# Optimization experiments

Hardware: AMD Instinct MI355X
Metric: run time of the kernel (lower is better)

The kernel has to match this reference:

```python
import jax, jax.numpy as jnp
import numpy as np

B, S, H, NH = 2, 2048, 1024, 16
PH = H // NH  # per-head size = 64


def setup_inputs() -> dict:
    key = jax.random.key(0)
    ks = jax.random.split(key, 12)
    scale = 0.02
    inp = {
        "key": jax.random.normal(ks[0], (B, S, H), jnp.float32),
        "value": jax.random.normal(ks[1], (B, S, H), jnp.float32),
        "query": jax.random.normal(ks[2], (B, S, H), jnp.float32),
        "mask": jax.random.uniform(ks[3], (B, 1, S, S), jnp.float32),
        "i": 0,
        "Wq": jax.random.normal(ks[4], (H, H), jnp.float32) * scale,
        "bq": jnp.zeros((H,), jnp.float32),
        "Wk": jax.random.normal(ks[5], (H, H), jnp.float32) * scale,
        "bk": jnp.zeros((H,), jnp.float32),
        "Wv": jax.random.normal(ks[6], (H, H), jnp.float32) * scale,
        "bv": jnp.zeros((H,), jnp.float32),
        "Wo": jax.random.normal(ks[7], (H, H), jnp.float32) * scale,
        "bo": jnp.zeros((H,), jnp.float32),
    }
    return inp


def reference(key, value, query, mask, i, Wq, bq, Wk, bk, Wv, bv, Wo, bo):
    # Linear projections (torch nn.Linear: x @ W.T + b), then split heads -> [B, NH, S, PH]
    def proj(x, W, b):
        return (x @ W.T + b).reshape(B, S, NH, PH).transpose(0, 2, 1, 3)

    q = proj(query, Wq, bq)
    k = proj(key, Wk, bk)
    v = proj(value, Wv, bv)

    # scores: [B, NH, S, S]; scale then MULTIPLICATIVE mask (as in the original)
    scores = jnp.einsum('bhqd,bhkd->bhqk', q, k) / jnp.sqrt(jnp.float32(PH))
    scores = scores * mask
    probs = jax.nn.softmax(scores, axis=-1)  # dropout p=0 -> identity

    # context: [B, NH, S, PH] -> merge heads -> [B, S, H]
    ctx = jnp.einsum('bhqk,bhkd->bhqd', probs, v)
    ctx = ctx.transpose(0, 2, 1, 3).reshape(B, S, H)
    return ctx @ Wo.T + bo
```

## Files before the change

### kernel.cpp

```cpp
#include <hip/hip_runtime.h>

typedef unsigned short ushort_t;
typedef __attribute__((ext_vector_type(8))) __bf16 bf16x8;
typedef __attribute__((ext_vector_type(4))) float f32x4;

__device__ inline float bf2f(ushort_t u) {
  union { unsigned int i; float f; } v; v.i = ((unsigned int)u) << 16; return v.f;
}
__device__ inline ushort_t f2bf(float f) {
  union { float f; unsigned int i; } v; v.f = f;
  unsigned int r = (v.i + 0x7fffu + ((v.i >> 16) & 1u)) >> 16;
  return (ushort_t)r;
}

__global__ void detect_dtype_kernel(const ushort_t* __restrict__ w,
                                    int* __restrict__ flag) {
  if (threadIdx.x == 0 && blockIdx.x == 0) {
    int sane = 0;
    for (int i = 0; i < 256; i++) {
      float a = fabsf(bf2f(w[i]));
      if (a >= 1e-4f && a <= 0.5f) sane++;
    }
    *flag = (sane >= 192) ? 1 : 0;
  }
}

__device__ inline float ld1(const void* src, size_t idx, int isbf) {
  return isbf ? bf2f(((const ushort_t*)src)[idx]) : ((const float*)src)[idx];
}

struct pre8 { float4 a, b; };
__device__ inline pre8 pref8(const void* src, size_t idx, int isbf) {
  pre8 u;
  if (isbf) {
    u.a = *(const float4*)((const ushort_t*)src + idx);
    u.b = u.a;
  } else {
    const float* s = (const float*)src + idx;
    u.a = *(const float4*)s;
    u.b = *(const float4*)(s + 4);
  }
  return u;
}
__device__ inline void commit8(ushort_t* dst, pre8 u, int isbf) {
  if (isbf) {
    *(float4*)dst = u.a;
  } else {
    union { bf16x8 v; ushort_t u8[8]; } t;
    t.u8[0] = f2bf(u.a.x); t.u8[1] = f2bf(u.a.y); t.u8[2] = f2bf(u.a.z); t.u8[3] = f2bf(u.a.w);
    t.u8[4] = f2bf(u.b.x); t.u8[5] = f2bf(u.b.y); t.u8[6] = f2bf(u.b.z); t.u8[7] = f2bf(u.b.w);
    *(bf16x8*)dst = t.v;
  }
}
__device__ inline void cvt8(ushort_t* dst, const void* src, size_t idx, int isbf) {
  commit8(dst, pref8(src, idx, isbf), isbf);
}

#define NW_ ((size_t)1024 * 1024)
#define NX_ ((size_t)4096 * 1024)
#define NM_ ((size_t)2 * 2048 * 2048)

__global__ __launch_bounds__(256) void cvt_all_kernel(
    const void* xq, const void* xk, const void* xv,
    const void* wq, const void* wk, const void* wv, const void* wo,
    const void* mask, ushort_t* __restrict__ dst,
    const int* __restrict__ flag) {
  int seg = blockIdx.z;
  const void* src; size_t n, doff;
  switch (seg) {
    case 0: src = wq;   n = NW_; doff = 0;                 break;
    case 1: src = wk;   n = NW_; doff = NW_;               break;
    case 2: src = wv;   n = NW_; doff = 2 * NW_;           break;
    case 3: src = wo;   n = NW_; doff = 3 * NW_;           break;
    case 4: src = xq;   n = NX_; doff = 4 * NW_;           break;
    case 5: src = xk;   n = NX_; doff = 4 * NW_ + NX_;     break;
    case 6: src = xv;   n = NX_; doff = 4 * NW_ + 2 * NX_; break;
    default: src = mask; n = NM_; doff = 4 * NW_ + 3 * NX_; break;
  }
  size_t i = ((size_t)blockIdx.x * 256 + threadIdx.x) * 8;
  if (i >= n) return;
  cvt8(&dst[doff + i], src, i, *flag);
}

#define KDIM 1024
#define NDIM 1024

__device__ __forceinline__ void gld_lds16(ushort_t* lds, const ushort_t* g) {
  __builtin_amdgcn_global_load_lds(
      (const __attribute__((address_space(1))) void*)g,
      (__attribute__((address_space(3))) void*)lds, 16, 0, 0);
}

template <int MODE>
__global__ __launch_bounds__(256) void gemm_fast_kernel(
    const ushort_t* __restrict__ X0, const ushort_t* __restrict__ X1,
    const ushort_t* __restrict__ X2,
    const ushort_t* __restrict__ W0, const ushort_t* __restrict__ W1,
    const ushort_t* __restrict__ W2,
    const void* __restrict__ B0, const void* __restrict__ B1,
    const void* __restrict__ B2,
    void* __restrict__ O0, void* __restrict__ O1, void* __restrict__ O2,
    const int* __restrict__ flag) {
  __shared__ ushort_t As[128 * 64];
  __shared__ ushort_t Bs[128 * 64];
  const int z = blockIdx.z;
  const ushort_t* X = z == 0 ? X0 : z == 1 ? X1 : X2;
  const ushort_t* W = z == 0 ? W0 : z == 1 ? W1 : W2;
  const void* Bias  = z == 0 ? B0 : z == 1 ? B1 : B2;
  void* Out         = z == 0 ? O0 : z == 1 ? O1 : O2;
  const int f = *flag;

  const int tid = threadIdx.x;
  const int wave = tid >> 6, lane = tid & 63;
  const int g = lane >> 4, l16 = lane & 15;
  const int m0 = blockIdx.y * 128, n0 = blockIdx.x * 128;
  const int wm = (wave >> 1) * 64, wn = (wave & 1) * 64;
  const int lr = lane >> 3;
  const int lc = (lane & 7) ^ lr;

  f32x4 acc[4][4] = {};

  for (int k0 = 0; k0 < KDIM; k0 += 64) {
#pragma unroll
    for (int q = 0; q < 4; q++) {
      const int row = wave * 32 + q * 8;
      gld_lds16(&As[row * 64],
                &X[(size_t)(m0 + row + lr) * KDIM + k0 + lc * 8]);
      gld_lds16(&Bs[row * 64],
                &W[(size_t)(n0 + row + lr) * KDIM + k0 + lc * 8]);
    }
    __syncthreads();

    bf16x8 af[2][4], bfr[2][4];
#pragma unroll
    for (int kk = 0; kk < 2; kk++)
#pragma unroll
      for (int i = 0; i < 4; i++) {
        const int cs = ((g + 4 * kk) ^ (l16 & 7)) * 8;
        af[kk][i]  = *(const bf16x8*)&As[(wm + i * 16 + l16) * 64 + cs];
        bfr[kk][i] = *(const bf16x8*)&Bs[(wn + i * 16 + l16) * 64 + cs];
      }
#pragma unroll
    for (int kk = 0; kk < 2; kk++)
#pragma unroll
      for (int i = 0; i < 4; i++)
#pragma unroll
        for (int j = 0; j < 4; j++)
          acc[i][j] = __builtin_amdgcn_mfma_f32_16x16x32_bf16(
              af[kk][i], bfr[kk][j], acc[i][j], 0, 0, 0);
    __syncthreads();
  }

  for (int i = 0; i < 4; i++)
    for (int j = 0; j < 4; j++)
      for (int r = 0; r < 4; r++) {
        int m = m0 + wm + i * 16 + g * 4 + r;
        int n = n0 + wn + j * 16 + l16;
        float v = acc[i][j][r] + ld1(Bias, n, f);
        if (MODE == 0) {
          if (f) ((ushort_t*)Out)[(size_t)m * NDIM + n] = f2bf(v);
          else   ((float*)Out)[(size_t)m * NDIM + n] = v;
        } else {
          int b = m >> 11, s = m & 2047, h = n >> 6, d = n & 63;
          ((ushort_t*)Out)[((((size_t)b * 16 + h) * 2048) + s) * 64 + d] = f2bf(v);
        }
      }
}

#define BK 32

template <int MODE>
__device__ inline void gemm_body(const void* __restrict__ X,
                                 const void* __restrict__ W,
                                 const void* __restrict__ Bias,
                                 void* __restrict__ Out,
                                 int xbf, int wbf, int bbf, int obf) {
  __shared__ ushort_t As[128][BK + 8];
  __shared__ ushort_t Bs[128][BK + 8];
  const int tid = threadIdx.x;
  const int wave = tid >> 6, lane = tid & 63;
  const int g = lane >> 4, l16 = lane & 15;
  const int m0 = blockIdx.y * 128, n0 = blockIdx.x * 128;
  const int wm = (wave >> 1) * 64, wn = (wave & 1) * 64;

  f32x4 acc[4][4] = {};
  const int r0 = tid >> 2, c0 = (tid & 3) * 8;
  const size_t ia0 = (size_t)(m0 + r0) * KDIM + c0;
  const size_t ia1 = (size_t)(m0 + r0 + 64) * KDIM + c0;
  const size_t ib0 = (size_t)(n0 + r0) * KDIM + c0;
  const size_t ib1 = (size_t)(n0 + r0 + 64) * KDIM + c0;

  pre8 pa0 = pref8(X, ia0, xbf), pa1 = pref8(X, ia1, xbf);
  pre8 pb0 = pref8(W, ib0, wbf), pb1 = pref8(W, ib1, wbf);

  for (int k0 = 0; k0 < KDIM; k0 += BK) {
    commit8(&As[r0][c0],      pa0, xbf);
    commit8(&As[r0 + 64][c0], pa1, xbf);
    commit8(&Bs[r0][c0],      pb0, wbf);
    commit8(&Bs[r0 + 64][c0], pb1, wbf);
    const int kn = (k0 + BK) & (KDIM - 1);
    pa0 = pref8(X, ia0 + kn, xbf); pa1 = pref8(X, ia1 + kn, xbf);
    pb0 = pref8(W, ib0 + kn, wbf); pb1 = pref8(W, ib1 + kn, wbf);
    __syncthreads();
    bf16x8 af[4], bfr[4];
    for (int i = 0; i < 4; i++) af[i]  = *(const bf16x8*)&As[wm + i * 16 + l16][g * 8];
    for (int j = 0; j < 4; j++) bfr[j] = *(const bf16x8*)&Bs[wn + j * 16 + l16][g * 8];
    for (int i = 0; i < 4; i++)
      for (int j = 0; j < 4; j++)
        acc[i][j] = __builtin_amdgcn_mfma_f32_16x16x32_bf16(af[i], bfr[j], acc[i][j], 0, 0, 0);
    __syncthreads();
  }
  for (int i = 0; i < 4; i++)
    for (int j = 0; j < 4; j++)
      for (int r = 0; r < 4; r++) {
        int m = m0 + wm + i * 16 + g * 4 + r;
        int n = n0 + wn + j * 16 + l16;
        float v = acc[i][j][r] + ld1(Bias, n, bbf);
        if (MODE == 0) {
          if (obf) ((ushort_t*)Out)[(size_t)m * NDIM + n] = f2bf(v);
          else     ((float*)Out)[(size_t)m * NDIM + n] = v;
        } else {
          int b = m >> 11, s = m & 2047, h = n >> 6, d = n & 63;
          ((ushort_t*)Out)[((((size_t)b * 16 + h) * 2048) + s) * 64 + d] = f2bf(v);
        }
      }
}

__global__ __launch_bounds__(256) void proj_qkv_fb_kernel(
    const void* __restrict__ query, const void* __restrict__ key,
    const void* __restrict__ value,
    const void* __restrict__ Wq, const void* __restrict__ bq,
    const void* __restrict__ Wk, const void* __restrict__ bk,
    const void* __restrict__ Wv, const void* __restrict__ bv,
    ushort_t* __restrict__ Q, ushort_t* __restrict__ K, ushort_t* __restrict__ V,
    const int* __restrict__ flag) {
  int f = *flag;
  int z = blockIdx.z;
  const void* X = z == 0 ? query : z == 1 ? key : value;
  const void* W = z == 0 ? Wq : z == 1 ? Wk : Wv;
  const void* B = z == 0 ? bq : z == 1 ? bk : bv;
  ushort_t* O  = z == 0 ? Q  : z == 1 ? K  : V;
  gemm_body<1>(X, W, B, O, f, f, f, 1);
}

__global__ __launch_bounds__(256) void out_proj_fb_kernel(
    const ushort_t* __restrict__ X, const void* __restrict__ W,
    const void* __restrict__ B, void* __restrict__ O,
    const int* __restrict__ flag) {
  int f = *flag;
  gemm_body<0>(X, W, B, O, 1, f, f, f);
}

__global__ __launch_bounds__(256) void transpose_v_kernel(
    const ushort_t* __restrict__ Vin, ushort_t* __restrict__ Vout) {
  __shared__ ushort_t T[64][72];
  const int tid = threadIdx.x;
  const int r = tid >> 2, c = (tid & 3) * 16;
  const int bh = blockIdx.y;
  const int s0 = blockIdx.x * 64;
  const ushort_t* src = Vin + (size_t)bh * 2048 * 64;
  *(bf16x8*)&T[r][c]     = *(const bf16x8*)&src[(size_t)(s0 + r) * 64 + c];
  *(bf16x8*)&T[r][c + 8] = *(const bf16x8*)&src[(size_t)(s0 + r) * 64 + c + 8];
  __syncthreads();
  union { bf16x8 v; ushort_t u[8]; } o0, o1;
  for (int i = 0; i < 8; i++) o0.u[i] = T[c + i][r];
  for (int i = 0; i < 8; i++) o1.u[i] = T[c + 8 + i][r];
  ushort_t* dst = Vout + (size_t)bh * 64 * 2048;
  *(bf16x8*)&dst[(size_t)r * 2048 + s0 + c]     = o0.v;
  *(bf16x8*)&dst[(size_t)r * 2048 + s0 + c + 8] = o1.v;
}

#define FS 72

template <int PRET>
__global__ __launch_bounds__(256, 4) void flash_attn_kernel(
    const ushort_t* __restrict__ Q, const ushort_t* __restrict__ K,
    const ushort_t* __restrict__ V, const void* __restrict__ mask,
    ushort_t* __restrict__ ctx, const int* __restrict__ flag, int convM) {
  __shared__ ushort_t QsM[64][FS];
  __shared__ ushort_t Ks[64][FS];
  __shared__ ushort_t Vs[64][FS];
  __shared__ ushort_t Ps[4][16][FS];

  const int mbf = convM ? 1 : *flag;
  const int tid = threadIdx.x;
  const int wave = tid >> 6, lane = tid & 63;
  const int g = lane >> 4, l16 = lane & 15;
  const int bh = blockIdx.x;
  const int b = bh >> 4, h = bh & 15;
  const int q0 = blockIdx.y * 64;

  const ushort_t* Qh = Q + (size_t)bh * 2048 * 64;
  const ushort_t* Kh = K + (size_t)bh * 2048 * 64;
  const ushort_t* Vh = PRET ? V + (size_t)bh * 64 * 2048
                            : V + (size_t)bh * 2048 * 64;
  const int mrow = wave * 16 + g * 4;
  const int r = tid >> 2, c = (tid & 3) * 16;
  const size_t mstage = (size_t)b * 2048 * 2048 + (size_t)(q0 + r) * 2048 + c;

  {
    union { bf16x8 v; ushort_t u[8]; } a0, a1;
    a0.v = *(const bf16x8*)&Qh[(size_t)(q0 + r) * 64 + c];
    a1.v = *(const bf16x8*)&Qh[(size_t)(q0 + r) * 64 + c + 8];
    for (int i = 0; i < 8; i++) {
      a0.u[i] = f2bf(bf2f(a0.u[i]) * 0.125f);
      a1.u[i] = f2bf(bf2f(a1.u[i]) * 0.125f);
    }
    *(bf16x8*)&QsM[r][c]     = a0.v;
    *(bf16x8*)&QsM[r][c + 8] = a1.v;
  }
  __syncthreads();
  const bf16x8 aq0 = *(const bf16x8*)&QsM[wave * 16 + l16][g * 8];
  const bf16x8 aq1 = *(const bf16x8*)&QsM[wave * 16 + l16][32 + g * 8];

  float lpart[4] = {0.f, 0.f, 0.f, 0.f};
  f32x4 o_acc[4] = {};

  bf16x8 kr0 = *(const bf16x8*)&Kh[(size_t)r * 64 + c];
  bf16x8 kr1 = *(const bf16x8*)&Kh[(size_t)r * 64 + c + 8];
  bf16x8 vr0, vr1;
  if (PRET) {
    vr0 = *(const bf16x8*)&Vh[(size_t)r * 2048 + c];
    vr1 = *(const bf16x8*)&Vh[(size_t)r * 2048 + c + 8];
  } else {
    vr0 = *(const bf16x8*)&Vh[(size_t)r * 64 + c];
    vr1 = *(const bf16x8*)&Vh[(size_t)r * 64 + c + 8];
  }
  pre8 pm0 = pref8(mask, mstage, mbf);
  pre8 pm1 = pref8(mask, mstage + 8, mbf);

  for (int kt0 = 0; kt0 < 2048; kt0 += 64) {
    __syncthreads();
    *(bf16x8*)&Ks[r][c]     = kr0;
    *(bf16x8*)&Ks[r][c + 8] = kr1;
    if (PRET) {
      *(bf16x8*)&Vs[r][c]     = vr0;
      *(bf16x8*)&Vs[r][c + 8] = vr1;
    } else {
      union { bf16x8 v; ushort_t u[8]; } a0, a1;
      a0.v = vr0; a1.v = vr1;
      for (int i = 0; i < 8; i++) Vs[c + i][r] = a0.u[i];
      for (int i = 0; i < 8; i++) Vs[c + 8 + i][r] = a1.u[i];
    }
    commit8(&QsM[r][c],     pm0, mbf);
    commit8(&QsM[r][c + 8], pm1, mbf);
    __syncthreads();

    const int ktn = (kt0 + 64) & 2047;
    bf16x8 nk0 = *(const bf16x8*)&Kh[(size_t)(ktn + r) * 64 + c];
    bf16x8 nk1 = *(const bf16x8*)&Kh[(size_t)(ktn + r) * 64 + c + 8];
    bf16x8 nv0, nv1;
    if (PRET) {
      nv0 = *(const bf16x8*)&Vh[(size_t)r * 2048 + ktn + c];
      nv1 = *(const bf16x8*)&Vh[(size_t)r * 2048 + ktn + c + 8];
    } else {
      nv0 = *(const bf16x8*)&Vh[(size_t)(ktn + r) * 64 + c];
      nv1 = *(const bf16x8*)&Vh[(size_t)(ktn + r) * 64 + c + 8];
    }
    pre8 nm0 = pref8(mask, mstage + ktn, mbf);
    pre8 nm1 = pref8(mask, mstage + ktn + 8, mbf);

    f32x4 sc[4] = {};
#pragma unroll
    for (int j = 0; j < 4; j++) {
      bf16x8 bk0 = *(const bf16x8*)&Ks[j * 16 + l16][g * 8];
      bf16x8 bk1 = *(const bf16x8*)&Ks[j * 16 + l16][32 + g * 8];
      sc[j] = __builtin_amdgcn_mfma_f32_16x16x32_bf16(aq0, bk0, sc[j], 0, 0, 0);
      sc[j] = __builtin_amdgcn_mfma_f32_16x16x32_bf16(aq1, bk1, sc[j], 0, 0, 0);
    }

#pragma unroll
    for (int j = 0; j < 4; j++)
#pragma unroll
      for (int rr = 0; rr < 4; rr++) {
        float m = bf2f(QsM[mrow + rr][j * 16 + l16]);
        float s = fminf(sc[j][rr] * m, 80.f);
        float p = __expf(s);
        unsigned int pb = __float_as_uint(p);
        lpart[rr] += __uint_as_float(pb & 0xffff0000u);
        Ps[wave][g * 4 + rr][j * 16 + l16] = (ushort_t)(pb >> 16);
      }
    asm volatile("" ::: "memory");

    bf16x8 pf0 = *(const bf16x8*)&Ps[wave][l16][g * 8];
    bf16x8 pf1 = *(const bf16x8*)&Ps[wave][l16][32 + g * 8];
#pragma unroll
    for (int jd = 0; jd < 4; jd++) {
      bf16x8 vf0 = *(const bf16x8*)&Vs[jd * 16 + l16][g * 8];
      bf16x8 vf1 = *(const bf16x8*)&Vs[jd * 16 + l16][32 + g * 8];
      o_acc[jd] = __builtin_amdgcn_mfma_f32_16x16x32_bf16(pf0, vf0, o_acc[jd], 0, 0, 0);
      o_acc[jd] = __builtin_amdgcn_mfma_f32_16x16x32_bf16(pf1, vf1, o_acc[jd], 0, 0, 0);
    }

    kr0 = nk0; kr1 = nk1; vr0 = nv0; vr1 = nv1;
    pm0 = nm0; pm1 = nm1;
  }

  float rl[4];
  for (int rr = 0; rr < 4; rr++) {
    float l = lpart[rr];
    l += __shfl_xor(l, 1, 64);
    l += __shfl_xor(l, 2, 64);
    l += __shfl_xor(l, 4, 64);
    l += __shfl_xor(l, 8, 64);
    rl[rr] = 1.0f / l;
  }
  for (int jd = 0; jd < 4; jd++)
    for (int rr = 0; rr < 4; rr++) {
      int qrow = q0 + mrow + rr;
      ctx[((size_t)b * 2048 + qrow) * 1024 + h * 64 + jd * 16 + l16] =
          f2bf(o_acc[jd][rr] * rl[rr]);
    }
}

extern "C" void kernel_launch(void* const* d_in, const int* in_sizes, int n_in,
                              void* d_out, int out_size, void* d_ws, size_t ws_size,
                              hipStream_t stream) {
  (void)in_sizes; (void)n_in; (void)out_size;
  const void* key   = d_in[0];
  const void* value = d_in[1];
  const void* query = d_in[2];
  const void* mask  = d_in[3];
  const void* Wq = d_in[5];
  const void* bq = d_in[6];
  const void* Wk = d_in[7];
  const void* bk = d_in[8];
  const void* Wv = d_in[9];
  const void* bv = d_in[10];
  const void* Wo = d_in[11];
  const void* bo = d_in[12];

  const size_t E = (size_t)2 * 2048 * 1024;
  ushort_t* Qw  = (ushort_t*)d_ws;
  ushort_t* Kw  = Qw + E;
  ushort_t* Vw  = Kw + E;
  ushort_t* CTX = Vw + E;
  int* flag = (int*)(CTX + E);
  ushort_t* Vt   = (ushort_t*)((char*)flag + 256);
  ushort_t* conv = Vt + E;

  const size_t need_pret = 4 * E * 2 + 256 + E * 2;
  const size_t need_W   = need_pret + 4 * NW_ * 2;
  const size_t need_WX  = need_W + 3 * NX_ * 2;
  const size_t need_all = need_WX + NM_ * 2;
  const int pret  = ws_size >= need_pret ? 1 : 0;
  const int convW = (pret && ws_size >= need_W)   ? 1 : 0;
  const int convX = (pret && ws_size >= need_WX)  ? 1 : 0;
  const int convM = (pret && ws_size >= need_all) ? 1 : 0;

  detect_dtype_kernel<<<1, 64, 0, stream>>>((const ushort_t*)Wq, flag);

  if (convW) {
    int nseg = convM ? 8 : (convX ? 7 : 4);
    int nx   = convM ? 4096 : (convX ? 2048 : 512);
    cvt_all_kernel<<<dim3(nx, 1, nseg), 256, 0, stream>>>(
        query, key, value, Wq, Wk, Wv, Wo, mask, conv, flag);
  }
  const ushort_t* Wq_c = conv;
  const ushort_t* Wk_c = conv + NW_;
  const ushort_t* Wv_c = conv + 2 * NW_;
  const ushort_t* Wo_c = conv + 3 * NW_;
  const ushort_t* Xq_c = conv + 4 * NW_;
  const ushort_t* Xk_c = conv + 4 * NW_ + NX_;
  const ushort_t* Xv_c = conv + 4 * NW_ + 2 * NX_;
  const void* M_e = convM ? (const void*)(conv + 4 * NW_ + 3 * NX_) : mask;

  if (convW && convX) {
    gemm_fast_kernel<1><<<dim3(8, 32, 3), 256, 0, stream>>>(
        Xq_c, Xk_c, Xv_c, Wq_c, Wk_c, Wv_c, bq, bk, bv,
        Qw, Kw, Vw, flag);
  } else {
    proj_qkv_fb_kernel<<<dim3(8, 32, 3), 256, 0, stream>>>(
        query, key, value, Wq, bq, Wk, bk, Wv, bv, Qw, Kw, Vw, flag);
  }

  if (pret) {
    transpose_v_kernel<<<dim3(32, 32), 256, 0, stream>>>(Vw, Vt);
    flash_attn_kernel<1><<<dim3(32, 32), 256, 0, stream>>>(Qw, Kw, Vt, M_e, CTX, flag, convM);
  } else {
    flash_attn_kernel<0><<<dim3(32, 32), 256, 0, stream>>>(Qw, Kw, Vw, M_e, CTX, flag, convM);
  }

  if (convW) {
    gemm_fast_kernel<0><<<dim3(8, 32, 1), 256, 0, stream>>>(
        CTX, CTX, CTX, Wo_c, Wo_c, Wo_c, bo, bo, bo,
        d_out, d_out, d_out, flag);
  } else {
    out_proj_fb_kernel<<<dim3(8, 32), 256, 0, stream>>>(CTX, Wo, bo, d_out, flag);
  }
}
```

Before: 343.2 us.

## Add 128-row query tile attention kernel with pre-transposed bf16 mask

Adds a flash-attention variant that processes 128 query rows per block (32 per wave), so each K/V tile loaded into LDS is reused across twice as many queries. The mask is converted and transposed into key-major bf16 layout by a new kernel, and the 1/sqrt(d) scale is folded into Q at load time. The dtype detection is also parallelised across a wavefront. The cost is more registers and LDS per block (occupancy hint lowered to 2), an extra transpose pass over the full mask, and extra rounding from pre-scaling Q in bf16.

```diff
diff --git a/kernel.cpp b/kernel.cpp
--- a/kernel.cpp
+++ b/kernel.cpp
@@ -2,6 +2,7 @@
 
 typedef unsigned short ushort_t;
 typedef __attribute__((ext_vector_type(8))) __bf16 bf16x8;
+typedef __attribute__((ext_vector_type(4))) __bf16 bf16x4;
 typedef __attribute__((ext_vector_type(4))) float f32x4;
 
 __device__ inline float bf2f(ushort_t u) {
@@ -15,14 +16,14 @@
 
 __global__ void detect_dtype_kernel(const ushort_t* __restrict__ w,
                                     int* __restrict__ flag) {
-  if (threadIdx.x == 0 && blockIdx.x == 0) {
-    int sane = 0;
-    for (int i = 0; i < 256; i++) {
-      float a = fabsf(bf2f(w[i]));
-      if (a >= 1e-4f && a <= 0.5f) sane++;
-    }
-    *flag = (sane >= 192) ? 1 : 0;
-  }
+  int lane = threadIdx.x & 63;
+  int cnt = 0;
+  for (int i = 0; i < 4; i++) {
+    float a = fabsf(bf2f(w[lane * 4 + i]));
+    if (a >= 1e-4f && a <= 0.5f) cnt++;
+  }
+  for (int off = 1; off < 64; off <<= 1) cnt += __shfl_xor(cnt, off, 64);
+  if (threadIdx.x == 0) *flag = (cnt >= 192) ? 1 : 0;
 }
 
 __device__ inline float ld1(const void* src, size_t idx, int isbf) {
@@ -63,23 +64,42 @@
 __global__ __launch_bounds__(256) void cvt_all_kernel(
     const void* xq, const void* xk, const void* xv,
     const void* wq, const void* wk, const void* wv, const void* wo,
-    const void* mask, ushort_t* __restrict__ dst,
-    const int* __restrict__ flag) {
+    ushort_t* __restrict__ dst, const int* __restrict__ flag) {
   int seg = blockIdx.z;
   const void* src; size_t n, doff;
   switch (seg) {
-    case 0: src = wq;   n = NW_; doff = 0;                 break;
-    case 1: src = wk;   n = NW_; doff = NW_;               break;
-    case 2: src = wv;   n = NW_; doff = 2 * NW_;           break;
-    case 3: src = wo;   n = NW_; doff = 3 * NW_;           break;
-    case 4: src = xq;   n = NX_; doff = 4 * NW_;           break;
-    case 5: src = xk;   n = NX_; doff = 4 * NW_ + NX_;     break;
-    case 6: src = xv;   n = NX_; doff = 4 * NW_ + 2 * NX_; break;
-    default: src = mask; n = NM_; doff = 4 * NW_ + 3 * NX_; break;
+    case 0: src = wq; n = NW_; doff = 0;                 break;
+    case 1: src = wk; n = NW_; doff = NW_;               break;
+    case 2: src = wv; n = NW_; doff = 2 * NW_;           break;
+    case 3: src = wo; n = NW_; doff = 3 * NW_;           break;
+    case 4: src = xq; n = NX_; doff = 4 * NW_;           break;
+    case 5: src = xk; n = NX_; doff = 4 * NW_ + NX_;     break;
+    default: src = xv; n = NX_; doff = 4 * NW_ + 2 * NX_; break;
   }
   size_t i = ((size_t)blockIdx.x * 256 + threadIdx.x) * 8;
   if (i >= n) return;
   cvt8(&dst[doff + i], src, i, *flag);
+}
+
+__global__ __launch_bounds__(256) void transpose_mask_kernel(
+    const void* __restrict__ M, ushort_t* __restrict__ Mt,
+    const int* __restrict__ flag) {
+  __shared__ ushort_t T[64][72];
+  const int f = *flag;
+  const int tid = threadIdx.x;
+  const int r = tid >> 2, c = (tid & 3) * 16;
+  const int b = blockIdx.z;
+  const int q0 = blockIdx.x * 64, k0 = blockIdx.y * 64;
+  const size_t src = (size_t)b * 2048 * 2048 + (size_t)(q0 + r) * 2048 + k0 + c;
+  cvt8(&T[r][c],     M, src, f);
+  cvt8(&T[r][c + 8], M, src + 8, f);
+  __syncthreads();
+  union { bf16x8 v; ushort_t u[8]; } o0, o1;
+  for (int i = 0; i < 8; i++) o0.u[i] = T[c + i][r];
+  for (int i = 0; i < 8; i++) o1.u[i] = T[c + 8 + i][r];
+  ushort_t* dst = Mt + (size_t)b * 2048 * 2048;
+  *(bf16x8*)&dst[(size_t)(k0 + r) * 2048 + q0 + c]     = o0.v;
+  *(bf16x8*)&dst[(size_t)(k0 + r) * 2048 + q0 + c + 8] = o1.v;
 }
 
 #define KDIM 1024
@@ -124,10 +144,8 @@
 #pragma unroll
     for (int q = 0; q < 4; q++) {
       const int row = wave * 32 + q * 8;
-      gld_lds16(&As[row * 64],
-                &X[(size_t)(m0 + row + lr) * KDIM + k0 + lc * 8]);
-      gld_lds16(&Bs[row * 64],
-                &W[(size_t)(n0 + row + lr) * KDIM + k0 + lc * 8]);
+      gld_lds16(&As[row * 64], &X[(size_t)(m0 + row + lr) * KDIM + k0 + lc * 8]);
+      gld_lds16(&Bs[row * 64], &W[(size_t)(n0 + row + lr) * KDIM + k0 + lc * 8]);
     }
     __syncthreads();
 
@@ -270,19 +288,162 @@
   *(bf16x8*)&dst[(size_t)r * 2048 + s0 + c + 8] = o1.v;
 }
 
+__global__ __launch_bounds__(256, 2) void flash_attn128_kernel(
+    const ushort_t* __restrict__ Q, const ushort_t* __restrict__ K,
+    const ushort_t* __restrict__ Vt, const ushort_t* __restrict__ Mt,
+    ushort_t* __restrict__ ctx) {
+  __shared__ ushort_t Ks[64 * 72];
+  __shared__ ushort_t Vs[64 * 72];
+  __shared__ ushort_t MQ[8448];
+  __shared__ ushort_t Ps[4][32 * 72];
+
+  const int tid = threadIdx.x;
+  const int wave = tid >> 6, lane = tid & 63;
+  const int g = lane >> 4, l16 = lane & 15;
+  const int bh = blockIdx.x;
+  const int b = bh >> 4, h = bh & 15;
+  const int q0 = blockIdx.y * 128;
+
+  const ushort_t* Qh = Q + (size_t)bh * 2048 * 64;
+  const ushort_t* Kh = K + (size_t)bh * 2048 * 64;
+  const ushort_t* Vh = Vt + (size_t)bh * 64 * 2048;
+  const ushort_t* Mh = Mt + (size_t)b * 2048 * 2048 + q0;
+
+  {
+    const int qr = tid >> 1, qc = (tid & 1) * 32;
+#pragma unroll
+    for (int ch = 0; ch < 4; ch++) {
+      union { bf16x8 v; ushort_t u[8]; } a;
+      a.v = *(const bf16x8*)&Qh[(size_t)(q0 + qr) * 64 + qc + ch * 8];
+      for (int i = 0; i < 8; i++) a.u[i] = f2bf(bf2f(a.u[i]) * 0.125f);
+      *(bf16x8*)&MQ[qr * 66 + qc + ch * 8] = a.v;
+    }
+  }
+  __syncthreads();
+  bf16x8 aq[2][2];
+#pragma unroll
+  for (int t = 0; t < 2; t++)
+#pragma unroll
+    for (int kk = 0; kk < 2; kk++)
+      aq[t][kk] = *(const bf16x8*)&MQ[(wave * 32 + t * 16 + l16) * 66 + kk * 32 + g * 8];
+
+  float lpart[2][4] = {};
+  f32x4 o_acc[2][4] = {};
+
+  const int r = tid >> 2, c = (tid & 3) * 16;
+  const int mc = (tid & 3) * 32;
+
+  bf16x8 kr0 = *(const bf16x8*)&Kh[(size_t)r * 64 + c];
+  bf16x8 kr1 = *(const bf16x8*)&Kh[(size_t)r * 64 + c + 8];
+  bf16x8 vr0 = *(const bf16x8*)&Vh[(size_t)r * 2048 + c];
+  bf16x8 vr1 = *(const bf16x8*)&Vh[(size_t)r * 2048 + c + 8];
+  bf16x8 pm0 = *(const bf16x8*)&Mh[(size_t)r * 2048 + mc];
+  bf16x8 pm1 = *(const bf16x8*)&Mh[(size_t)r * 2048 + mc + 8];
+  bf16x8 pm2 = *(const bf16x8*)&Mh[(size_t)r * 2048 + mc + 16];
+  bf16x8 pm3 = *(const bf16x8*)&Mh[(size_t)r * 2048 + mc + 24];
+
+  for (int kt0 = 0; kt0 < 2048; kt0 += 64) {
+    __syncthreads();
+    *(bf16x8*)&Ks[r * 72 + c]      = kr0;
+    *(bf16x8*)&Ks[r * 72 + c + 8]  = kr1;
+    *(bf16x8*)&Vs[r * 72 + c]      = vr0;
+    *(bf16x8*)&Vs[r * 72 + c + 8]  = vr1;
+    *(bf16x8*)&MQ[r * 132 + mc]      = pm0;
+    *(bf16x8*)&MQ[r * 132 + mc + 8]  = pm1;
+    *(bf16x8*)&MQ[r * 132 + mc + 16] = pm2;
+    *(bf16x8*)&MQ[r * 132 + mc + 24] = pm3;
+    __syncthreads();
+
+    const int ktn = (kt0 + 64) & 2047;
+    kr0 = *(const bf16x8*)&Kh[(size_t)(ktn + r) * 64 + c];
+    kr1 = *(const bf16x8*)&Kh[(size_t)(ktn + r) * 64 + c + 8];
+    vr0 = *(const bf16x8*)&Vh[(size_t)r * 2048 + ktn + c];
+    vr1 = *(const bf16x8*)&Vh[(size_t)r * 2048 + ktn + c + 8];
+    pm0 = *(const bf16x8*)&Mh[(size_t)(ktn + r) * 2048 + mc];
+    pm1 = *(const bf16x8*)&Mh[(size_t)(ktn + r) * 2048 + mc + 8];
+    pm2 = *(const bf16x8*)&Mh[(size_t)(ktn + r) * 2048 + mc + 16];
+    pm3 = *(const bf16x8*)&Mh[(size_t)(ktn + r) * 2048 + mc + 24];
+
+    f32x4 sc[2][4] = {};
+#pragma unroll
+    for (int j = 0; j < 4; j++) {
+      bf16x8 bk0 = *(const bf16x8*)&Ks[(j * 16 + l16) * 72 + g * 8];
+      bf16x8 bk1 = *(const bf16x8*)&Ks[(j * 16 + l16) * 72 + 32 + g * 8];
+#pragma unroll
+      for (int t = 0; t < 2; t++) {
+        sc[t][j] = __builtin_amdgcn_mfma_f32_16x16x32_bf16(aq[t][0], bk0, sc[t][j], 0, 0, 0);
+        sc[t][j] = __builtin_amdgcn_mfma_f32_16x16x32_bf16(aq[t][1], bk1, sc[t][j], 0, 0, 0);
+      }
+    }
+
+#pragma unroll
+    for (int t = 0; t < 2; t++)
+#pragma unroll
+      for (int j = 0; j < 4; j++) {
+        union { bf16x4 v; ushort_t u[4]; } m4;
+        m4.v = *(const bf16x4*)&MQ[(j * 16 + l16) * 132 + wave * 32 + t * 16 + g * 4];
+#pragma unroll
+        for (int rr = 0; rr < 4; rr++) {
+          float s = fminf(sc[t][j][rr] * bf2f(m4.u[rr]), 80.f);
+          float p = __expf(s);
+          unsigned int pb = __float_as_uint(p);
+          lpart[t][rr] += __uint_as_float(pb & 0xffff0000u);
+          Ps[wave][(t * 16 + g * 4 + rr) * 72 + j * 16 + l16] = (ushort_t)(pb >> 16);
+        }
+      }
+    asm volatile("" ::: "memory");
+
+    bf16x8 pf00 = *(const bf16x8*)&Ps[wave][(l16) * 72 + g * 8];
+    bf16x8 pf01 = *(const bf16x8*)&Ps[wave][(l16) * 72 + 32 + g * 8];
+    bf16x8 pf10 = *(const bf16x8*)&Ps[wave][(16 + l16) * 72 + g * 8];
+    bf16x8 pf11 = *(const bf16x8*)&Ps[wave][(16 + l16) * 72 + 32 + g * 8];
+#pragma unroll
+    for (int jd = 0; jd < 4; jd++) {
+      bf16x8 vf0 = *(const bf16x8*)&Vs[(jd * 16 + l16) * 72 + g * 8];
+      bf16x8 vf1 = *(const bf16x8*)&Vs[(jd * 16 + l16) * 72 + 32 + g * 8];
+      o_acc[0][jd] = __builtin_amdgcn_mfma_f32_16x16x32_bf16(pf00, vf0, o_acc[0][jd], 0, 0, 0);
+      o_acc[0][jd] = __builtin_amdgcn_mfma_f32_16x16x32_bf16(pf01, vf1, o_acc[0][jd], 0, 0, 0);
+      o_acc[1][jd] = __builtin_amdgcn_mfma_f32_16x16x32_bf16(pf10, vf0, o_acc[1][jd], 0, 0, 0);
+      o_acc[1][jd] = __builtin_amdgcn_mfma_f32_16x16x32_bf16(pf11, vf1, o_acc[1][jd], 0, 0, 0);
+    }
+  }
+
+#pragma unroll
+  for (int t = 0; t < 2; t++) {
+    float rl[4];
+#pragma unroll
+    for (int rr = 0; rr < 4; rr++) {
+      float l = lpart[t][rr];
+      l += __shfl_xor(l, 1, 64);
+      l += __shfl_xor(l, 2, 64);
+      l += __shfl_xor(l, 4, 64);
+      l += __shfl_xor(l, 8, 64);
+      rl[rr] = 1.0f / l;
+    }
+#pragma unroll
+    for (int jd = 0; jd < 4; jd++)
+#pragma unroll
+      for (int rr = 0; rr < 4; rr++) {
+        int qrow = q0 + wave * 32 + t * 16 + g * 4 + rr;
+        ctx[((size_t)b * 2048 + qrow) * 1024 + h * 64 + jd * 16 + l16] =
+            f2bf(o_acc[t][jd][rr] * rl[rr]);
+      }
+  }
+}
+
 #define FS 72
 
 template <int PRET>
 __global__ __launch_bounds__(256, 4) void flash_attn_kernel(
     const ushort_t* __restrict__ Q, const ushort_t* __restrict__ K,
     const ushort_t* __restrict__ V, const void* __restrict__ mask,
-    ushort_t* __restrict__ ctx, const int* __restrict__ flag, int convM) {
+    ushort_t* __restrict__ ctx, const int* __restrict__ flag) {
   __shared__ ushort_t QsM[64][FS];
   __shared__ ushort_t Ks[64][FS];
   __shared__ ushort_t Vs[64][FS];
   __shared__ ushort_t Ps[4][16][FS];
 
-  const int mbf = convM ? 1 : *flag;
+  const int mbf = *flag;
   const int tid = threadIdx.x;
   const int wave = tid >> 6, lane = tid & 63;
   const int g = lane >> 4, l16 = lane & 15;
@@ -347,18 +508,17 @@
     __syncthreads();
 
     const int ktn = (kt0 + 64) & 2047;
-    bf16x8 nk0 = *(const bf16x8*)&Kh[(size_t)(ktn + r) * 64 + c];
-    bf16x8 nk1 = *(const bf16x8*)&Kh[(size_t)(ktn + r) * 64 + c + 8];
-    bf16x8 nv0, nv1;
+    kr0 = *(const bf16x8*)&Kh[(size_t)(ktn + r) * 64 + c];
+    kr1 = *(const bf16x8*)&Kh[(size_t)(ktn + r) * 64 + c + 8];
     if (PRET) {
-      nv0 = *(const bf16x8*)&Vh[(size_t)r * 2048 + ktn + c];
-      nv1 = *(const bf16x8*)&Vh[(size_t)r * 2048 + ktn + c + 8];
+      vr0 = *(const bf16x8*)&Vh[(size_t)r * 2048 + ktn + c];
+      vr1 = *(const bf16x8*)&Vh[(size_t)r * 2048 + ktn + c + 8];
     } else {
-      nv0 = *(const bf16x8*)&Vh[(size_t)(ktn + r) * 64 + c];
-      nv1 = *(const bf16x8*)&Vh[(size_t)(ktn + r) * 64 + c + 8];
-    }
-    pre8 nm0 = pref8(mask, mstage + ktn, mbf);
-    pre8 nm1 = pref8(mask, mstage + ktn + 8, mbf);
+      vr0 = *(const bf16x8*)&Vh[(size_t)(ktn + r) * 64 + c];
+      vr1 = *(const bf16x8*)&Vh[(size_t)(ktn + r) * 64 + c + 8];
+    }
+    pm0 = pref8(mask, mstage + ktn, mbf);
+    pm1 = pref8(mask, mstage + ktn + 8, mbf);
 
     f32x4 sc[4] = {};
 #pragma unroll
@@ -391,9 +551,6 @@
       o_acc[jd] = __builtin_amdgcn_mfma_f32_16x16x32_bf16(pf0, vf0, o_acc[jd], 0, 0, 0);
       o_acc[jd] = __builtin_amdgcn_mfma_f32_16x16x32_bf16(pf1, vf1, o_acc[jd], 0, 0, 0);
     }
-
-    kr0 = nk0; kr1 = nk1; vr0 = nv0; vr1 = nv1;
-    pm0 = nm0; pm1 = nm1;
   }
 
   float rl[4];
@@ -451,10 +608,10 @@
   detect_dtype_kernel<<<1, 64, 0, stream>>>((const ushort_t*)Wq, flag);
 
   if (convW) {
-    int nseg = convM ? 8 : (convX ? 7 : 4);
-    int nx   = convM ? 4096 : (convX ? 2048 : 512);
+    int nseg = convX ? 7 : 4;
+    int nx   = convX ? 2048 : 512;
     cvt_all_kernel<<<dim3(nx, 1, nseg), 256, 0, stream>>>(
-        query, key, value, Wq, Wk, Wv, Wo, mask, conv, flag);
+        query, key, value, Wq, Wk, Wv, Wo, conv, flag);
   }
   const ushort_t* Wq_c = conv;
   const ushort_t* Wk_c = conv + NW_;
@@ -463,7 +620,11 @@
   const ushort_t* Xq_c = conv + 4 * NW_;
   const ushort_t* Xk_c = conv + 4 * NW_ + NX_;
   const ushort_t* Xv_c = conv + 4 * NW_ + 2 * NX_;
-  const void* M_e = convM ? (const void*)(conv + 4 * NW_ + 3 * NX_) : mask;
+  ushort_t* Mt = conv + 4 * NW_ + 3 * NX_;
+
+  if (convM) {
+    transpose_mask_kernel<<<dim3(32, 32, 2), 256, 0, stream>>>(mask, Mt, flag);
+  }
 
   if (convW && convX) {
     gemm_fast_kernel<1><<<dim3(8, 32, 3), 256, 0, stream>>>(
@@ -476,9 +637,13 @@
 
   if (pret) {
     transpose_v_kernel<<<dim3(32, 32), 256, 0, stream>>>(Vw, Vt);
-    flash_attn_kernel<1><<<dim3(32, 32), 256, 0, stream>>>(Qw, Kw, Vt, M_e, CTX, flag, convM);
+    if (convM) {
+      flash_attn128_kernel<<<dim3(32, 16), 256, 0, stream>>>(Qw, Kw, Vt, Mt, CTX);
+    } else {
+      flash_attn_kernel<1><<<dim3(32, 32), 256, 0, stream>>>(Qw, Kw, Vt, mask, CTX, flag);
+    }
   } else {
-    flash_attn_kernel<0><<<dim3(32, 32), 256, 0, stream>>>(Qw, Kw, Vw, M_e, CTX, flag, convM);
+    flash_attn_kernel<0><<<dim3(32, 32), 256, 0, stream>>>(Qw, Kw, Vw, mask, CTX, flag);
   }
 
   if (convW) {
```

Measured after the change: 330.1 us. 1.04x faster.
